# Kernel tuning notes

Hardware: AMD Instinct MI355X
Metric: run time of the kernel (lower is better)

The kernel has to match this reference:

```python
import jax, jax.numpy as jnp
import numpy as np

N_NODES = 100000
N_EDGES = 3200000
IN_F, HID, OUT_F = 512, 64, 64
K_HOPS = 10


def setup_inputs() -> dict:
    key = jax.random.key(0)
    k1, k2, k3, k4, k5 = jax.random.split(key, 5)
    x = jax.random.normal(k1, (N_NODES, IN_F), dtype=jnp.float32)
    edge_index = jax.random.randint(k2, (2, N_EDGES), 0, N_NODES, dtype=jnp.int64)
    # Glorot-ish scaled params (bias=False per init_kwargs)
    W1 = jax.random.normal(k3, (IN_F, HID), dtype=jnp.float32) / np.sqrt(IN_F)
    W2 = jax.random.normal(k4, (HID, OUT_F), dtype=jnp.float32) / np.sqrt(HID)
    s = jax.random.normal(k5, (OUT_F, 1), dtype=jnp.float32) / np.sqrt(OUT_F)
    return {"x": x, "edge_index": edge_index, "W1": W1, "W2": W2, "s": s}


def reference(x, edge_index, W1, W2, s):
    # --- MLP (dropout omitted: eval mode), relu applied after each linear per source ---
    h = jnp.maximum(x @ W1, 0.0)          # [N, HID]
    h = jnp.maximum(h @ W2, 0.0)          # [N, OUT_F]

    src = edge_index[0]
    dst = edge_index[1]
    n = h.shape[0]
    ones = jnp.ones(src.shape[0], dtype=h.dtype)
    deg_out = jax.ops.segment_sum(ones, src, num_segments=n)
    deg_in = jax.ops.segment_sum(ones, dst, num_segments=n)
    dinv_out = jnp.where(deg_out > 0, jax.lax.rsqrt(jnp.maximum(deg_out, 1.0)), 0.0)
    dinv_in = jnp.where(deg_in > 0, jax.lax.rsqrt(jnp.maximum(deg_in, 1.0)), 0.0)
    norm = dinv_out[src] * dinv_in[dst]   # [E] symmetric normalization

    # --- K-hop propagation: D^{-1/2} A D^{-1/2} applied K times ---
    hops = [h]
    feat = h
    for _ in range(K_HOPS):  # small fixed K, unrolled
        msg = feat[src] * norm[:, None]                          # gather [E, F]
        feat = jax.ops.segment_sum(msg, dst, num_segments=n)     # scatter [N, F]
        hops.append(feat)
    H = jnp.stack(hops, axis=1)            # [N, K+1, F]

    # --- adaptive hop combination via sigmoid gate ---
    scores = jax.nn.sigmoid(H @ s)         # [N, K+1, 1]
    out = jnp.sum(scores * H, axis=1)      # [N, F]
    return out
```

## Files before the change

### kernel.cpp

```cpp
#include <hip/hip_runtime.h>
#include <hip/hip_bf16.h>

#define N_NODES 100000
#define N_EDGES 3200000
#define IN_F 512
#define HID 64
#define OUT_F 64
#define K_HOPS 10

#define HIST_BLOCKS 64
#define HIST_BINS 32768
#define HIST_WORDS (HIST_BINS / 2)
#define EDGES_PER_HIST_BLOCK (N_EDGES / HIST_BLOCKS)

#define NBKT 224
#define NBN  448
#define BKT_CAP 16384
#define BKZ_BLOCKS 256
#define EDGES_PER_BKZ_BLOCK (N_EDGES / BKZ_BLOCKS)
#define BKZ_BATCH 8192

typedef __attribute__((ext_vector_type(8))) short bf16x8;
typedef __attribute__((ext_vector_type(4))) float f32x4;

static __device__ __forceinline__ unsigned short f2bf(float f) {
    unsigned int u = __float_as_uint(f);
    u += 0x7FFFu + ((u >> 16) & 1u);
    return (unsigned short)(u >> 16);
}
static __device__ __forceinline__ float bf2f(unsigned short s) {
    return __uint_as_float(((unsigned int)s) << 16);
}

__global__ void detect_i32_kernel(const unsigned int* ei_words, int* flag_is32) {
    int i = blockIdx.x * blockDim.x + threadIdx.x;
    unsigned int w = ei_words[2 * i + 1];
    if (w != 0u) atomicOr(flag_is32, 1);
}

__global__ void __launch_bounds__(256) convert_kernel(const void* ei_raw, const int* flag_is32,
                                                      int* __restrict__ src32,
                                                      int* __restrict__ dst32) {
    int t = blockIdx.x * blockDim.x + threadIdx.x;
    if (t >= N_EDGES / 2) return;
    if (*flag_is32) {
        const int2* ei = (const int2*)ei_raw;
        *(int2*)(src32 + 2 * t) = ei[t];
        *(int2*)(dst32 + 2 * t) = ei[N_EDGES / 2 + t];
    } else {
        const longlong2* ei = (const longlong2*)ei_raw;
        longlong2 s = ei[t];
        longlong2 d = ei[N_EDGES / 2 + t];
        *(int2*)(src32 + 2 * t) = make_int2((int)s.x, (int)s.y);
        *(int2*)(dst32 + 2 * t) = make_int2((int)d.x, (int)d.y);
    }
}

__global__ void __launch_bounds__(256) wconv_kernel(const float* __restrict__ W1,
                                                    const float* __restrict__ W2,
                                                    unsigned short* __restrict__ b1g,
                                                    unsigned short* __restrict__ b2g) {
    int o = blockIdx.x * blockDim.x + threadIdx.x;
    int which = (o >= IN_F * HID);
    int oo = which ? (o - IN_F * HID) : o;
    int ko = oo & 7;
    int l = (oo >> 3) & 63;
    int kgs = l >> 4;
    int cm = l & 15;
    int tile = oo >> 9;
    int gt = tile >> 2;
    int nt = tile & 3;
    int k = gt * 32 + kgs * 8 + ko;
    int c = nt * 16 + cm;
    if (which) b2g[oo] = f2bf(W2[k * OUT_F + c]);
    else       b1g[oo] = f2bf(W1[k * HID + c]);
}

__global__ void __launch_bounds__(256) hist_kernel(const int* __restrict__ a,
                                                   unsigned int* __restrict__ partials) {
    __shared__ unsigned int cnt[HIST_WORDS];
    int tid = threadIdx.x;
    for (int w = tid; w < HIST_WORDS; w += 256) cnt[w] = 0u;
    __syncthreads();

    int range = blockIdx.y;
    unsigned lo = (unsigned)(range * HIST_BINS);
    int beg = blockIdx.x * EDGES_PER_HIST_BLOCK;
    int end = beg + EDGES_PER_HIST_BLOCK;
    for (int i = beg + tid; i < end; i += 256) {
        unsigned v = (unsigned)a[i] - lo;
        if (v < HIST_BINS) atomicAdd(&cnt[v >> 1], 1u << ((v & 1u) * 16u));
    }
    __syncthreads();

    unsigned int* outp = partials + ((size_t)(blockIdx.y * HIST_BLOCKS + blockIdx.x)) * HIST_WORDS;
    for (int w = tid; w < HIST_WORDS / 4; w += 256)
        ((uint4*)outp)[w] = ((const uint4*)cnt)[w];
}

__global__ void __launch_bounds__(256) hist_scan_kernel(const unsigned int* __restrict__ partials,
                                                        float* __restrict__ dinv) {
    int wg = blockIdx.x * blockDim.x + threadIdx.x;
    if (wg >= 4 * HIST_WORDS) return;
    int range = wg >> 14;
    int word = wg & (HIST_WORDS - 1);
    const unsigned int* base = partials + ((size_t)range * HIST_BLOCKS) * HIST_WORDS + word;
    unsigned lo = 0, hi = 0;
    for (int b = 0; b < HIST_BLOCKS; ++b) {
        unsigned c = base[(size_t)b * HIST_WORDS];
        lo += c & 0xffffu;
        hi += c >> 16;
    }
    int v0 = range * HIST_BINS + 2 * word;
    if (v0 < N_NODES) dinv[v0] = lo ? rsqrtf((float)lo) : 0.0f;
    int v1 = v0 + 1;
    if (v1 < N_NODES) dinv[v1] = hi ? rsqrtf((float)hi) : 0.0f;
}

__global__ void __launch_bounds__(256) bucket_cnt_kernel(const int* __restrict__ dst32,
                                                         int* __restrict__ bucket_cnt) {
    __shared__ int c[NBKT];
    int tid = threadIdx.x;
    if (tid < NBKT) c[tid] = 0;
    __syncthreads();
    int beg = blockIdx.x * EDGES_PER_BKZ_BLOCK;
    int end = beg + EDGES_PER_BKZ_BLOCK;
    for (int i = beg + tid; i < end; i += 256) {
        atomicAdd(&c[dst32[i] / NBN], 1);
    }
    __syncthreads();
    if (tid < NBKT && c[tid] > 0) atomicAdd(&bucket_cnt[tid], c[tid]);
}

__global__ void __launch_bounds__(256) bucket_scan_kernel(const int* __restrict__ bucket_cnt,
                                                          int* __restrict__ bucket_start,
                                                          int* __restrict__ gcur,
                                                          int* __restrict__ row_start) {
    __shared__ int s[256];
    int t = threadIdx.x;
    int c = (t < NBKT) ? bucket_cnt[t] : 0;
    s[t] = c;
    __syncthreads();
    for (int off = 1; off < 256; off <<= 1) {
        int add = (t >= off) ? s[t - off] : 0;
        __syncthreads();
        s[t] += add;
        __syncthreads();
    }
    if (t < NBKT) {
        int excl = s[t] - c;
        bucket_start[t] = excl;
        gcur[t] = excl;
        if (t == NBKT - 1) {
            bucket_start[NBKT] = s[t];
            row_start[N_NODES] = s[t];
        }
    }
}

__global__ void __launch_bounds__(256) bucketize_kernel(const int* __restrict__ src32,
                                                        const int* __restrict__ dst32,
                                                        int* __restrict__ gcur,
                                                        int* __restrict__ entries) {
    __shared__ unsigned int stag[BKZ_BATCH];
    __shared__ unsigned char stagb[BKZ_BATCH];
    __shared__ int cnt[256], sAr[256], ofs_l[256], gbase_l[256];

    int tid = threadIdx.x;
    int beg = blockIdx.x * EDGES_PER_BKZ_BLOCK;

    for (int bb = 0; bb < EDGES_PER_BKZ_BLOCK; bb += BKZ_BATCH) {
        int bn = min(BKZ_BATCH, EDGES_PER_BKZ_BLOCK - bb);
        cnt[tid] = 0;
        __syncthreads();

        unsigned pk[32];
#pragma unroll
        for (int j = 0; j < 32; ++j) {
            int loc = j * 256 + tid;
            pk[j] = 0xFFFFFFFFu;
            if (loc < bn) {
                int d = dst32[beg + bb + loc];
                int b = d / NBN;
                int dl = d - b * NBN;
                int off = atomicAdd(&cnt[b], 1);
                pk[j] = ((unsigned)b << 22) | ((unsigned)dl << 13) | (unsigned)off;
            }
        }
        __syncthreads();
        int c = cnt[tid];
        sAr[tid] = c;
        __syncthreads();
        for (int off = 1; off < 256; off <<= 1) {
            int add = (tid >= off) ? sAr[tid - off] : 0;
            __syncthreads();
            sAr[tid] += add;
            __syncthreads();
        }
        ofs_l[tid] = sAr[tid] - c;
        if (tid < NBKT && c > 0) gbase_l[tid] = atomicAdd(&gcur[tid], c);
        __syncthreads();

#pragma unroll
        for (int j = 0; j < 32; ++j) {
            int loc = j * 256 + tid;
            if (loc < bn && pk[j] != 0xFFFFFFFFu) {
                int s = src32[beg + bb + loc];
                int b = pk[j] >> 22;
                int dl = (pk[j] >> 13) & 511;
                int off = pk[j] & 8191;
                int pos = ofs_l[b] + off;
                stag[pos] = ((unsigned)s << 9) | (unsigned)dl;
                stagb[pos] = (unsigned char)b;
            }
        }
        __syncthreads();
        for (int i = tid; i < bn; i += 256) {
            int b = stagb[i];
            entries[gbase_l[b] + (i - ofs_l[b])] = (int)stag[i];
        }
        __syncthreads();
    }
}

#define SORT_LDS_BYTES ((2 * BKT_CAP + 512 + 512) * 4)
__global__ void __launch_bounds__(1024) sort_kernel(const int* __restrict__ entries,
                                                    const int* __restrict__ bucket_start,
                                                    int* __restrict__ srcs,
                                                    int* __restrict__ row_start,
                                                    float* __restrict__ dinv_in) {
    extern __shared__ int sbuf[];
    int* sin  = sbuf;
    int* sout = sbuf + BKT_CAP;
    int* cnt  = sbuf + 2 * BKT_CAP;
    int* nsum = cnt + 512;
    int tid = threadIdx.x;
    int b = blockIdx.x;
    int ebeg = bucket_start[b];
    int eend = bucket_start[b + 1];
    int n = eend - ebeg;

    for (int i = tid; i < n; i += 1024) sin[i] = entries[ebeg + i];
    if (tid < 512) { cnt[tid] = 0; nsum[tid] = 0; }
    __syncthreads();
    for (int i = tid; i < n; i += 1024) {
        atomicAdd(&cnt[(unsigned)sin[i] & 511u], 1);
    }
    __syncthreads();
    int c = (tid < 512) ? cnt[tid] : 0;
    if (tid < 512) nsum[tid] = c;
    __syncthreads();
    for (int off = 1; off < 512; off <<= 1) {
        int v = (tid < 512 && tid >= off) ? nsum[tid - off] : 0;
        __syncthreads();
        if (tid < 512) nsum[tid] += v;
        __syncthreads();
    }
    if (tid < NBN) {
        int excl = nsum[tid] - c;
        cnt[tid] = excl;
        int node = b * NBN + tid;
        if (node < N_NODES) {
            row_start[node] = ebeg + excl;
            dinv_in[node] = c ? rsqrtf((float)c) : 0.0f;
        }
    }
    __syncthreads();
    for (int i = tid; i < n; i += 1024) {
        unsigned e = (unsigned)sin[i];
        int pos = atomicAdd(&cnt[e & 511u], 1);
        sout[pos] = (int)(e >> 9);
    }
    __syncthreads();
    for (int i = tid; i < n; i += 1024) srcs[ebeg + i] = sout[i];
}

__global__ void __launch_bounds__(256) mlp_kernel(const float* __restrict__ x,
                                                  const unsigned short* __restrict__ b1g,
                                                  const unsigned short* __restrict__ b2g,
                                                  const float* __restrict__ dinv_out,
                                                  unsigned short* __restrict__ g0) {
    __shared__ __align__(16) unsigned short a2s[4][2 * 64 * 8];

    int tid = threadIdx.x;
    int w = tid >> 6;
    int l = tid & 63;
    int kg = l >> 4;
    int m  = l & 15;
    int row0 = blockIdx.x * 64;
    int row = row0 + w * 16 + m;
    bool valid = row < N_NODES;
    const float* xp = x + (size_t)row * IN_F + kg * 8;

    f32x4 acc[4];
#pragma unroll
    for (int nt = 0; nt < 4; ++nt) acc[nt] = (f32x4){0.f, 0.f, 0.f, 0.f};

#pragma unroll 4
    for (int gt = 0; gt < 16; ++gt) {
        union { bf16x8 v; unsigned short u[8]; } a;
        if (valid) {
            const float* ap = xp + gt * 32;
            float4 u0 = *(const float4*)ap;
            float4 u1 = *(const float4*)(ap + 4);
            a.u[0] = f2bf(u0.x); a.u[1] = f2bf(u0.y);
            a.u[2] = f2bf(u0.z); a.u[3] = f2bf(u0.w);
            a.u[4] = f2bf(u1.x); a.u[5] = f2bf(u1.y);
            a.u[6] = f2bf(u1.z); a.u[7] = f2bf(u1.w);
        } else {
#pragma unroll
            for (int q = 0; q < 8; ++q) a.u[q] = 0;
        }
#pragma unroll
        for (int nt = 0; nt < 4; ++nt) {
            bf16x8 b = *(const bf16x8*)&b1g[((gt * 4 + nt) * 64 + l) * 8];
            acc[nt] = __builtin_amdgcn_mfma_f32_16x16x32_bf16(a.v, b, acc[nt], 0, 0, 0);
        }
    }

#pragma unroll
    for (int nt = 0; nt < 4; ++nt) {
#pragma unroll
        for (int reg = 0; reg < 4; ++reg) {
            float v = fmaxf(acc[nt][reg], 0.0f);
            int cc = nt * 16 + m;
            int r = kg * 4 + reg;
            a2s[w][((cc >> 5) * 64 + (((cc >> 3) & 3) * 16 + r)) * 8 + (cc & 7)] = f2bf(v);
        }
    }

    f32x4 acc2[4];
#pragma unroll
    for (int nt = 0; nt < 4; ++nt) acc2[nt] = (f32x4){0.f, 0.f, 0.f, 0.f};
#pragma unroll
    for (int t2 = 0; t2 < 2; ++t2) {
        bf16x8 a = *(const bf16x8*)&a2s[w][(t2 * 64 + l) * 8];
#pragma unroll
        for (int nt = 0; nt < 4; ++nt) {
            bf16x8 b = *(const bf16x8*)&b2g[((t2 * 4 + nt) * 64 + l) * 8];
            acc2[nt] = __builtin_amdgcn_mfma_f32_16x16x32_bf16(a, b, acc2[nt], 0, 0, 0);
        }
    }

#pragma unroll
    for (int reg = 0; reg < 4; ++reg) {
        int node = row0 + w * 16 + kg * 4 + reg;
        if (node < N_NODES) {
            float dv = dinv_out[node];
#pragma unroll
            for (int nt = 0; nt < 4; ++nt) {
                g0[(size_t)node * OUT_F + nt * 16 + m] =
                    f2bf(dv * fmaxf(acc2[nt][reg], 0.0f));
            }
        }
    }
}

__global__ void __launch_bounds__(256) hop_kernel(
        const unsigned short* __restrict__ g_prev,
        const int* __restrict__ row_start,
        const int* __restrict__ srcs,
        const float* __restrict__ dinv_in,
        const float* __restrict__ dinv_out,
        unsigned short* __restrict__ g_next) {
    int lane = threadIdx.x & 63;
    int node = blockIdx.x * 4 + (threadIdx.x >> 6);
    if (node >= N_NODES) return;
    int beg = row_start[node];
    int end = row_start[node + 1];
    int slot = lane >> 3;
    int sub  = lane & 7;

    float acc[8];
#pragma unroll
    for (int j = 0; j < 8; ++j) acc[j] = 0.0f;

    for (int chunk = beg; chunk < end; chunk += 64) {
        int nrem = end - chunk;
        int es = (chunk + lane < end) ? srcs[chunk + lane] : 0;

        uint4 v[8];
#pragma unroll
        for (int g = 0; g < 8; ++g) {
            int s = __shfl(es, g * 8 + slot, 64);
            if (g * 8 + slot < nrem)
                v[g] = *(const uint4*)(g_prev + (size_t)s * OUT_F + sub * 8);
        }
#pragma unroll
        for (int g = 0; g < 8; ++g) {
            if (g * 8 + slot < nrem) {
                acc[0] += __uint_as_float(v[g].x << 16);
                acc[1] += __uint_as_float(v[g].x & 0xffff0000u);
                acc[2] += __uint_as_float(v[g].y << 16);
                acc[3] += __uint_as_float(v[g].y & 0xffff0000u);
                acc[4] += __uint_as_float(v[g].z << 16);
                acc[5] += __uint_as_float(v[g].z & 0xffff0000u);
                acc[6] += __uint_as_float(v[g].w << 16);
                acc[7] += __uint_as_float(v[g].w & 0xffff0000u);
            }
        }
    }
#pragma unroll
    for (int off = 8; off <= 32; off <<= 1) {
#pragma unroll
        for (int j = 0; j < 8; ++j) acc[j] += __shfl_xor(acc[j], off, 64);
    }
    if (slot == 0) {
        float sc = dinv_in[node] * dinv_out[node];
        uint4 wv;
        wv.x = (unsigned)f2bf(sc * acc[0]) | ((unsigned)f2bf(sc * acc[1]) << 16);
        wv.y = (unsigned)f2bf(sc * acc[2]) | ((unsigned)f2bf(sc * acc[3]) << 16);
        wv.z = (unsigned)f2bf(sc * acc[4]) | ((unsigned)f2bf(sc * acc[5]) << 16);
        wv.w = (unsigned)f2bf(sc * acc[6]) | ((unsigned)f2bf(sc * acc[7]) << 16);
        *(uint4*)(g_next + (size_t)node * OUT_F + sub * 8) = wv;
    }
}

__global__ void __launch_bounds__(256) combine_kernel(
        const unsigned short* __restrict__ garena,
        const float* __restrict__ dinv_out,
        const float* __restrict__ sv,
        float* __restrict__ out) {
    int lane = threadIdx.x & 63;
    int node = blockIdx.x * 4 + (threadIdx.x >> 6);
    if (node >= N_NODES) return;
    float dv = dinv_out[node];
    float rinv = (dv > 0.0f) ? 1.0f / dv : 0.0f;
    float sl = sv[lane];
    size_t idx = (size_t)node * OUT_F + lane;
    const size_t gstride = (size_t)N_NODES * OUT_F;

    float o = 0.0f;
#pragma unroll
    for (int k = 0; k <= K_HOPS; ++k) {
        float fn = bf2f(garena[(size_t)k * gstride + idx]) * rinv;
        float p = fn * sl;
#pragma unroll
        for (int off = 1; off <= 32; off <<= 1) p += __shfl_xor(p, off, 64);
        float score = 1.0f / (1.0f + expf(-p));
        o = fmaf(score, fn, o);
    }
    out[idx] = o;
}

extern "C" void kernel_launch(void* const* d_in, const int* in_sizes, int n_in,
                              void* d_out, int out_size, void* d_ws, size_t ws_size,
                              hipStream_t stream) {
    const float* x  = (const float*)d_in[0];
    const void*  ei = d_in[1];
    const float* W1 = (const float*)d_in[2];
    const float* W2 = (const float*)d_in[3];
    const float* sv = (const float*)d_in[4];
    float* out = (float*)d_out;

    char* p = (char*)d_ws;
    auto alloc = [&](size_t bytes) -> char* {
        char* r = p;
        p += (bytes + 255) & ~(size_t)255;
        return r;
    };
    const size_t gstride = (size_t)N_NODES * OUT_F;
    unsigned short* garena = (unsigned short*)alloc(sizeof(unsigned short) * gstride * (K_HOPS + 1));
    int*   src32     = (int*)alloc(sizeof(int) * N_EDGES);
    int*   dst32     = (int*)alloc(sizeof(int) * N_EDGES);
    char*  shared_region = alloc(sizeof(unsigned int) * 4 * HIST_BLOCKS * HIST_WORDS);
    unsigned int* partials = (unsigned int*)shared_region;
    int*   entries_raw = (int*)shared_region;
    int*   srcs      = (int*)alloc(sizeof(int) * N_EDGES);
    unsigned short* b1g = (unsigned short*)alloc(sizeof(unsigned short) * IN_F * HID);
    unsigned short* b2g = (unsigned short*)alloc(sizeof(unsigned short) * HID * OUT_F);
    float* dinv_out  = (float*)alloc(sizeof(float) * N_NODES);
    float* dinv_in   = (float*)alloc(sizeof(float) * N_NODES);
    int*   row_start = (int*)alloc(sizeof(int) * (N_NODES + 1));
    int*   bucket_cnt   = (int*)alloc(sizeof(int) * NBKT);
    int*   bucket_start = (int*)alloc(sizeof(int) * (NBKT + 1));
    int*   gcur      = (int*)alloc(sizeof(int) * NBKT);
    int*   flag      = (int*)alloc(256);

    hipMemsetAsync(flag, 0, sizeof(int), stream);
    hipMemsetAsync(bucket_cnt, 0, sizeof(int) * NBKT, stream);

    detect_i32_kernel<<<4, 256, 0, stream>>>((const unsigned int*)ei, flag);
    convert_kernel<<<(N_EDGES / 2 + 255) / 256, 256, 0, stream>>>(ei, flag, src32, dst32);
    wconv_kernel<<<(IN_F * HID + HID * OUT_F + 255) / 256, 256, 0, stream>>>(W1, W2, b1g, b2g);

    hist_kernel<<<dim3(HIST_BLOCKS, 4), 256, 0, stream>>>(src32, partials);
    hist_scan_kernel<<<(4 * HIST_WORDS + 255) / 256, 256, 0, stream>>>(partials, dinv_out);

    bucket_cnt_kernel<<<BKZ_BLOCKS, 256, 0, stream>>>(dst32, bucket_cnt);
    bucket_scan_kernel<<<1, 256, 0, stream>>>(bucket_cnt, bucket_start, gcur, row_start);
    bucketize_kernel<<<BKZ_BLOCKS, 256, 0, stream>>>(src32, dst32, gcur, entries_raw);

    hipFuncSetAttribute((const void*)sort_kernel,
                        hipFuncAttributeMaxDynamicSharedMemorySize, SORT_LDS_BYTES);
    sort_kernel<<<NBKT, 1024, SORT_LDS_BYTES, stream>>>(entries_raw, bucket_start,
                                                        srcs, row_start, dinv_in);

    int mlp_blocks = (N_NODES + 63) / 64;
    mlp_kernel<<<mlp_blocks, 256, 0, stream>>>(x, b1g, b2g, dinv_out, garena);

    int node_blocks = (N_NODES + 3) / 4;
    for (int hop = 1; hop <= K_HOPS; ++hop) {
        hop_kernel<<<node_blocks, 256, 0, stream>>>(garena + (size_t)(hop - 1) * gstride,
                                                    row_start, srcs, dinv_in, dinv_out,
                                                    garena + (size_t)hop * gstride);
    }
    combine_kernel<<<node_blocks, 256, 0, stream>>>(garena, dinv_out, sv, out);
}
```

Before: 799.9 us.

## Process two nodes per wavefront in hop kernel and fuse bucket counting into convert

```diff
diff --git a/kernel.cpp b/kernel.cpp
--- a/kernel.cpp
+++ b/kernel.cpp
@@ -38,22 +38,42 @@
     if (w != 0u) atomicOr(flag_is32, 1);
 }
 
-__global__ void __launch_bounds__(256) convert_kernel(const void* ei_raw, const int* flag_is32,
-                                                      int* __restrict__ src32,
-                                                      int* __restrict__ dst32) {
-    int t = blockIdx.x * blockDim.x + threadIdx.x;
-    if (t >= N_EDGES / 2) return;
-    if (*flag_is32) {
-        const int2* ei = (const int2*)ei_raw;
-        *(int2*)(src32 + 2 * t) = ei[t];
-        *(int2*)(dst32 + 2 * t) = ei[N_EDGES / 2 + t];
-    } else {
-        const longlong2* ei = (const longlong2*)ei_raw;
-        longlong2 s = ei[t];
-        longlong2 d = ei[N_EDGES / 2 + t];
-        *(int2*)(src32 + 2 * t) = make_int2((int)s.x, (int)s.y);
-        *(int2*)(dst32 + 2 * t) = make_int2((int)d.x, (int)d.y);
-    }
+__global__ void __launch_bounds__(256) convert_cnt_kernel(const void* ei_raw,
+                                                          const int* flag_is32,
+                                                          int* __restrict__ src32,
+                                                          int* __restrict__ dst32,
+                                                          int* __restrict__ bucket_cnt) {
+    __shared__ int c[NBKT];
+    int tid = threadIdx.x;
+    if (tid < NBKT) c[tid] = 0;
+    __syncthreads();
+    const int pairs = EDGES_PER_BKZ_BLOCK / 2;
+    int base = blockIdx.x * pairs;
+    int is32 = *flag_is32;
+    for (int it = 0; it < pairs; it += 256) {
+        int loc = it + tid;
+        if (loc < pairs) {
+            int t = base + loc;
+            int2 sp, dp;
+            if (is32) {
+                const int2* ei = (const int2*)ei_raw;
+                sp = ei[t];
+                dp = ei[N_EDGES / 2 + t];
+            } else {
+                const longlong2* ei = (const longlong2*)ei_raw;
+                longlong2 s = ei[t];
+                longlong2 d = ei[N_EDGES / 2 + t];
+                sp = make_int2((int)s.x, (int)s.y);
+                dp = make_int2((int)d.x, (int)d.y);
+            }
+            *(int2*)(src32 + 2 * t) = sp;
+            *(int2*)(dst32 + 2 * t) = dp;
+            atomicAdd(&c[dp.x / NBN], 1);
+            atomicAdd(&c[dp.y / NBN], 1);
+        }
+    }
+    __syncthreads();
+    if (tid < NBKT && c[tid] > 0) atomicAdd(&bucket_cnt[tid], c[tid]);
 }
 
 __global__ void __launch_bounds__(256) wconv_kernel(const float* __restrict__ W1,
@@ -117,21 +137,6 @@
     if (v1 < N_NODES) dinv[v1] = hi ? rsqrtf((float)hi) : 0.0f;
 }
 
-__global__ void __launch_bounds__(256) bucket_cnt_kernel(const int* __restrict__ dst32,
-                                                         int* __restrict__ bucket_cnt) {
-    __shared__ int c[NBKT];
-    int tid = threadIdx.x;
-    if (tid < NBKT) c[tid] = 0;
-    __syncthreads();
-    int beg = blockIdx.x * EDGES_PER_BKZ_BLOCK;
-    int end = beg + EDGES_PER_BKZ_BLOCK;
-    for (int i = beg + tid; i < end; i += 256) {
-        atomicAdd(&c[dst32[i] / NBN], 1);
-    }
-    __syncthreads();
-    if (tid < NBKT && c[tid] > 0) atomicAdd(&bucket_cnt[tid], c[tid]);
-}
-
 __global__ void __launch_bounds__(256) bucket_scan_kernel(const int* __restrict__ bucket_cnt,
                                                           int* __restrict__ bucket_start,
                                                           int* __restrict__ gcur,
@@ -364,31 +369,33 @@
         const float* __restrict__ dinv_out,
         unsigned short* __restrict__ g_next) {
     int lane = threadIdx.x & 63;
-    int node = blockIdx.x * 4 + (threadIdx.x >> 6);
+    int h = lane & 31;
+    int node = blockIdx.x * 8 + ((threadIdx.x >> 6) << 1) + (lane >> 5);
     if (node >= N_NODES) return;
     int beg = row_start[node];
     int end = row_start[node + 1];
-    int slot = lane >> 3;
-    int sub  = lane & 7;
+    int slot = h >> 3;
+    int sub  = h & 7;
+    int hbase = lane & 32;
 
     float acc[8];
 #pragma unroll
     for (int j = 0; j < 8; ++j) acc[j] = 0.0f;
 
-    for (int chunk = beg; chunk < end; chunk += 64) {
+    for (int chunk = beg; chunk < end; chunk += 32) {
         int nrem = end - chunk;
-        int es = (chunk + lane < end) ? srcs[chunk + lane] : 0;
+        int es = (chunk + h < end) ? srcs[chunk + h] : 0;
 
         uint4 v[8];
 #pragma unroll
         for (int g = 0; g < 8; ++g) {
-            int s = __shfl(es, g * 8 + slot, 64);
-            if (g * 8 + slot < nrem)
+            int s = __shfl(es, hbase + g * 4 + slot, 64);
+            if (g * 4 + slot < nrem)
                 v[g] = *(const uint4*)(g_prev + (size_t)s * OUT_F + sub * 8);
         }
 #pragma unroll
         for (int g = 0; g < 8; ++g) {
-            if (g * 8 + slot < nrem) {
+            if (g * 4 + slot < nrem) {
                 acc[0] += __uint_as_float(v[g].x << 16);
                 acc[1] += __uint_as_float(v[g].x & 0xffff0000u);
                 acc[2] += __uint_as_float(v[g].y << 16);
@@ -401,7 +408,7 @@
         }
     }
 #pragma unroll
-    for (int off = 8; off <= 32; off <<= 1) {
+    for (int off = 8; off <= 16; off <<= 1) {
 #pragma unroll
         for (int j = 0; j < 8; ++j) acc[j] += __shfl_xor(acc[j], off, 64);
     }
@@ -481,13 +488,12 @@
     hipMemsetAsync(bucket_cnt, 0, sizeof(int) * NBKT, stream);
 
     detect_i32_kernel<<<4, 256, 0, stream>>>((const unsigned int*)ei, flag);
-    convert_kernel<<<(N_EDGES / 2 + 255) / 256, 256, 0, stream>>>(ei, flag, src32, dst32);
+    convert_cnt_kernel<<<BKZ_BLOCKS, 256, 0, stream>>>(ei, flag, src32, dst32, bucket_cnt);
     wconv_kernel<<<(IN_F * HID + HID * OUT_F + 255) / 256, 256, 0, stream>>>(W1, W2, b1g, b2g);
 
     hist_kernel<<<dim3(HIST_BLOCKS, 4), 256, 0, stream>>>(src32, partials);
     hist_scan_kernel<<<(4 * HIST_WORDS + 255) / 256, 256, 0, stream>>>(partials, dinv_out);
 
-    bucket_cnt_kernel<<<BKZ_BLOCKS, 256, 0, stream>>>(dst32, bucket_cnt);
     bucket_scan_kernel<<<1, 256, 0, stream>>>(bucket_cnt, bucket_start, gcur, row_start);
     bucketize_kernel<<<BKZ_BLOCKS, 256, 0, stream>>>(src32, dst32, gcur, entries_raw);
 
@@ -499,11 +505,12 @@
     int mlp_blocks = (N_NODES + 63) / 64;
     mlp_kernel<<<mlp_blocks, 256, 0, stream>>>(x, b1g, b2g, dinv_out, garena);
 
+    int hop_blocks = (N_NODES + 7) / 8;
+    for (int hop = 1; hop <= K_HOPS; ++hop) {
+        hop_kernel<<<hop_blocks, 256, 0, stream>>>(garena + (size_t)(hop - 1) * gstride,
+                                                   row_start, srcs, dinv_in, dinv_out,
+                                                   garena + (size_t)hop * gstride);
+    }
     int node_blocks = (N_NODES + 3) / 4;
-    for (int hop = 1; hop <= K_HOPS; ++hop) {
-        hop_kernel<<<node_blocks, 256, 0, stream>>>(garena + (size_t)(hop - 1) * gstride,
-                                                    row_start, srcs, dinv_in, dinv_out,
-                                                    garena + (size_t)hop * gstride);
-    }
     combine_kernel<<<node_blocks, 256, 0, stream>>>(garena, dinv_out, sv, out);
 }
```

After: 759.9 us. 1.05x faster.
